# Optimization experiments

Measured on AMD Instinct MI355X. Metric: run time of the kernel, lower is better.

Reference implementation:

```python
import jax, jax.numpy as jnp
import numpy as np
import math

CHANNELS = 1024
NUM_HEADS = 16
HEAD_DIM = CHANNELS // NUM_HEADS  # 64
ROPE_DIM = int(HEAD_DIM * 0.5)    # 32
BASE_FREQ = 10000.0


def apply_rope(x):
    """x: [b, h, t, d]; rotate first ROPE_DIM features, pass the rest through."""
    t = x.shape[2]
    half = ROPE_DIM // 2
    theta = 1.0 / (BASE_FREQ ** (jnp.arange(0, ROPE_DIM, 2, dtype=jnp.float32) / ROPE_DIM))  # [half]
    ang = jnp.arange(t, dtype=jnp.float32)[:, None] * theta[None, :]  # [t, half]
    ang = jnp.concatenate([ang, ang], axis=-1)  # [t, ROPE_DIM]
    cos = jnp.cos(ang)[None, None, :, :]
    sin = jnp.sin(ang)[None, None, :, :]
    x_rope, x_pass = x[..., :ROPE_DIM], x[..., ROPE_DIM:]
    neg_half = jnp.concatenate([-x_rope[..., half:], x_rope[..., :half]], axis=-1)
    x_rope = x_rope * cos + neg_half * sin
    return jnp.concatenate([x_rope, x_pass], axis=-1)


def proximal_bias(length):
    pos = jnp.arange(length, dtype=jnp.float32)
    diff = pos[None, :] - pos[:, None]
    return -jnp.log1p(jnp.abs(diff))[None, None, :, :]  # [1,1,t,t]


def conv1x1(x, w, b):
    """x: [b, c_in, t], w: [c_out, c_in], b: [c_out] -> [b, c_out, t]"""
    return jnp.einsum('oc,bct->bot', w, x) + b[None, :, None]


def setup_inputs() -> dict:
    key = jax.random.key(0)
    ks = jax.random.split(key, 10)
    B, C, T = 8, CHANNELS, 1024
    scale = 1.0 / math.sqrt(C)
    return {
        "x": jax.random.normal(ks[0], (B, C, T), dtype=jnp.float32),
        "context": jax.random.normal(ks[1], (B, C, T), dtype=jnp.float32),
        "attention_mask": jnp.ones((B, 1, 1, T), dtype=jnp.int32),
        "Wq": jax.random.normal(ks[2], (C, C), dtype=jnp.float32) * scale,
        "bq": jnp.zeros((C,), dtype=jnp.float32),
        "Wk": jax.random.normal(ks[3], (C, C), dtype=jnp.float32) * scale,
        "bk": jnp.zeros((C,), dtype=jnp.float32),
        "Wv": jax.random.normal(ks[4], (C, C), dtype=jnp.float32) * scale,
        "bv": jnp.zeros((C,), dtype=jnp.float32),
        "Wo": jax.random.normal(ks[5], (C, C), dtype=jnp.float32) * scale,
        "bo": jnp.zeros((C,), dtype=jnp.float32),
    }


def reference(x, context, attention_mask, Wq, bq, Wk, bk, Wv, bv, Wo, bo):
    B, C, T = x.shape
    H, D = NUM_HEADS, HEAD_DIM
    q = conv1x1(x, Wq, bq)
    k = conv1x1(context, Wk, bk)
    v = conv1x1(context, Wv, bv)
    # b (h d) t -> b h t d
    def split_heads(z):
        return z.reshape(B, H, D, -1).transpose(0, 1, 3, 2)
    q, k, v = split_heads(q), split_heads(k), split_heads(v)
    q = apply_rope(q)
    k = apply_rope(k)
    scores = jnp.einsum('bhqd,bhkd->bhqk', q, k) / math.sqrt(D)
    scores = scores + proximal_bias(T)  # proximal_bias=True, self-attention
    scores = jnp.where(attention_mask == 0, jnp.float32(-10000.0), scores)
    probs = jax.nn.softmax(scores, axis=-1)  # dropout_rate=0.0 -> identity
    out = jnp.einsum('bhqk,bhkd->bhqd', probs, v)
    # b h q d -> b (h d) q
    out = out.transpose(0, 1, 3, 2).reshape(B, C, T)
    return conv1x1(out, Wo, bo)
```

## Files before the change

kernel.cpp:

```cpp
#include <hip/hip_runtime.h>
#include <hip/hip_bf16.h>
#include <math.h>

#define BB 8
#define CC 1024
#define TT 1024
#define HH 16
#define DD 64

typedef __attribute__((ext_vector_type(8))) short short8;
typedef __attribute__((ext_vector_type(4))) short short4_;
typedef __attribute__((ext_vector_type(4))) float f32x4;
typedef __attribute__((ext_vector_type(4))) int   i32x4;
typedef __attribute__((ext_vector_type(2))) unsigned long long u64x2;

#define QSCALE 0.18033688f

__device__ __forceinline__ unsigned short f2bf(float f) {
    unsigned u = __builtin_bit_cast(unsigned, f);
    u += 0x7fffu + ((u >> 16) & 1u);
    return (unsigned short)(u >> 16);
}

__device__ __forceinline__ f32x4 mfma16(short8 a, short8 b, f32x4 c) {
    return __builtin_amdgcn_mfma_f32_16x16x32_bf16(a, b, c, 0, 0, 0);
}

__device__ __forceinline__ void async16(const void* g, void* l) {
    __builtin_amdgcn_global_load_lds(
        (const __attribute__((address_space(1))) unsigned int*)g,
        (__attribute__((address_space(3))) unsigned int*)l, 16, 0, 0);
}

__device__ __forceinline__ unsigned cvtpk(float lo, float hi) {
    unsigned r;
    asm("v_cvt_pk_bf16_f32 %0, %1, %2" : "=v"(r) : "v"(lo), "v"(hi));
    return r;
}

__device__ __forceinline__ short8 vfrag(const short* p) {
    u64x2 t;
    t[0] = *(const unsigned long long*)(p);
    t[1] = *(const unsigned long long*)(p + 16);
    return __builtin_bit_cast(short8, t);
}

__global__ __launch_bounds__(256) void cast_w_kernel(
    const float* __restrict__ Wq, const float* __restrict__ Wk,
    const float* __restrict__ Wv, const float* __restrict__ Wo,
    unsigned short* __restrict__ dst)
{
    const int z = blockIdx.y;
    const float* W = (z == 0) ? Wq : (z == 1) ? Wk : (z == 2) ? Wv : Wo;
    unsigned short* d = dst + (size_t)z * CC * CC;
    int idx = blockIdx.x * 256 + threadIdx.x;
    float4 f = ((const float4*)W)[idx];
    short4_ s;
    s[0] = (short)f2bf(f.x); s[1] = (short)f2bf(f.y);
    s[2] = (short)f2bf(f.z); s[3] = (short)f2bf(f.w);
    ((short4_*)d)[idx] = s;
}

__global__ __launch_bounds__(256) void tcast2_kernel(
    const float* __restrict__ x, const float* __restrict__ ctx,
    unsigned short* __restrict__ xT, unsigned short* __restrict__ cTo)
{
    __shared__ float sT[64][65];
    const int tid = threadIdx.x;
    const int z = blockIdx.z;
    const float* in = (z < BB) ? x : ctx;
    unsigned short* out = (z < BB) ? xT : cTo;
    const int b = (z < BB) ? z : z - BB;
    const int tB = blockIdx.x * 64, cT = blockIdx.y * 64;

    const float* ib = in + ((size_t)b * CC + cT) * TT + tB;
    const int r = tid >> 2;
    #pragma unroll
    for (int j = 0; j < 4; j++) {
        int t4 = (tid & 3) * 4 + j * 16;
        float4 f = *(const float4*)(ib + (size_t)r * TT + t4);
        sT[r][t4 + 0] = f.x; sT[r][t4 + 1] = f.y;
        sT[r][t4 + 2] = f.z; sT[r][t4 + 3] = f.w;
    }
    __syncthreads();
    const int t_l = tid >> 2, cch = (tid & 3) * 16;
    short8 o0, o1;
    #pragma unroll
    for (int i = 0; i < 8; i++) {
        o0[i] = (short)f2bf(sT[cch + i][t_l]);
        o1[i] = (short)f2bf(sT[cch + 8 + i][t_l]);
    }
    unsigned short* dp = out + ((size_t)b * TT + tB + t_l) * CC + cT + cch;
    *(short8*)dp = o0;
    *(short8*)(dp + 8) = o1;
}

__global__ __launch_bounds__(256) void tcast_kernel(
    const float* __restrict__ in, unsigned short* __restrict__ out)
{
    __shared__ float sT[64][65];
    const int tid = threadIdx.x;
    const int tB = blockIdx.x * 64, cT = blockIdx.y * 64, b = blockIdx.z;

    const float* ib = in + ((size_t)b * CC + cT) * TT + tB;
    const int r = tid >> 2;
    #pragma unroll
    for (int j = 0; j < 4; j++) {
        int t4 = (tid & 3) * 4 + j * 16;
        float4 f = *(const float4*)(ib + (size_t)r * TT + t4);
        sT[r][t4 + 0] = f.x; sT[r][t4 + 1] = f.y;
        sT[r][t4 + 2] = f.z; sT[r][t4 + 3] = f.w;
    }
    __syncthreads();
    const int t_l = tid >> 2, cch = (tid & 3) * 16;
    short8 o0, o1;
    #pragma unroll
    for (int i = 0; i < 8; i++) {
        o0[i] = (short)f2bf(sT[cch + i][t_l]);
        o1[i] = (short)f2bf(sT[cch + 8 + i][t_l]);
    }
    unsigned short* dp = out + ((size_t)b * TT + tB + t_l) * CC + cT + cch;
    *(short8*)dp = o0;
    *(short8*)(dp + 8) = o1;
}

__global__ __launch_bounds__(256) void qkv_gll_kernel(
    const unsigned short* __restrict__ xT, const unsigned short* __restrict__ cT,
    const unsigned short* __restrict__ Wq2, const unsigned short* __restrict__ Wk2,
    const unsigned short* __restrict__ Wv2,
    const float* __restrict__ bq, const float* __restrict__ bk,
    const float* __restrict__ bv,
    unsigned short* __restrict__ qo, unsigned short* __restrict__ ko,
    unsigned short* __restrict__ vo,
    int mode)
{
    __shared__ __align__(16) short smem[4 * 64 * 72];
    short* sA = smem;
    short* sB = smem + 4096;

    const int tid = threadIdx.x, lane = tid & 63, wave = tid >> 6;
    const int wm = wave >> 1, wn = wave & 1;
    const int l15 = lane & 15, lq = lane >> 4;

    const int tTile = blockIdx.x, oTile = blockIdx.y;
    const int zz = blockIdx.z;
    int w, b;
    if (mode == 0)      { w = zz % 3;        b = zz / 3;  }
    else if (mode == 1) { w = 0;             b = zz;      }
    else                { w = 1 + (zz & 1);  b = zz >> 1; }
    const unsigned short* inT = (w == 0) ? xT : cT;
    const int oBase = oTile * 128, tBase = tTile * 128;

    const unsigned short* WA = (w == 0) ? Wq2 : (w == 1) ? Wk2 : Wv2;
    const float* bias        = (w == 0) ? bq  : (w == 1) ? bk  : bv;

    const int srow = lane >> 2;
    const int sch  = (lane ^ (lane >> 2) ^ (lane >> 4)) & 3;
    const unsigned short* gA0 = WA + (size_t)(oBase + wave * 32 + srow) * CC + sch * 8;
    const unsigned short* gA1 = gA0 + (size_t)16 * CC;
    const unsigned short* gB0 = inT + ((size_t)b * TT + tBase + wave * 32 + srow) * CC + sch * 8;
    const unsigned short* gB1 = gB0 + (size_t)16 * CC;
    short* lA0 = sA + (wave * 2 + 0) * 512;
    short* lA1 = sA + (wave * 2 + 1) * 512;
    short* lB0 = sB + (wave * 2 + 0) * 512;
    short* lB1 = sB + (wave * 2 + 1) * 512;

    const int csw = ((lq ^ (l15 & 3) ^ (l15 >> 2)) & 3) * 8;

    f32x4 acc[4][4];
    #pragma unroll
    for (int mt = 0; mt < 4; mt++)
        #pragma unroll
        for (int nt = 0; nt < 4; nt++) acc[mt][nt] = (f32x4){0.f, 0.f, 0.f, 0.f};

    for (int c0 = 0; c0 < CC; c0 += 32) {
        async16(gA0 + c0, lA0);
        async16(gA1 + c0, lA1);
        async16(gB0 + c0, lB0);
        async16(gB1 + c0, lB1);
        __syncthreads();

        short8 af[4], bf[4];
        #pragma unroll
        for (int mt = 0; mt < 4; mt++)
            af[mt] = *(short8*)(sA + (wm * 64 + mt * 16 + l15) * 32 + csw);
        #pragma unroll
        for (int nt = 0; nt < 4; nt++)
            bf[nt] = *(short8*)(sB + (wn * 64 + nt * 16 + l15) * 32 + csw);
        #pragma unroll
        for (int mt = 0; mt < 4; mt++)
            #pragma unroll
            for (int nt = 0; nt < 4; nt++)
                acc[mt][nt] = mfma16(af[mt], bf[nt], acc[mt][nt]);
        __syncthreads();
    }

    #pragma unroll
    for (int mt = 0; mt < 4; mt++)
        #pragma unroll
        for (int r = 0; r < 4; r++) {
            float bi = bias[oBase + wm * 64 + mt * 16 + lq * 4 + r];
            #pragma unroll
            for (int nt = 0; nt < 4; nt++) {
                acc[mt][nt][r] += bi;
                if (w == 0) acc[mt][nt][r] *= QSCALE;
            }
        }

    const int h = oTile * 2 + wm;
    short* sT = smem + wave * (64 * 72);

    if (w < 2) {
        #pragma unroll
        for (int r = 0; r < 4; r++) {
            float dr = (float)(lq * 4 + r);
            float theta = exp2f(dr * -0.8304820237f);
            float sa, ca, ss, cs;
            sincosf((float)(tBase + wn * 64 + l15) * theta, &sa, &ca);
            sincosf(16.0f * theta, &ss, &cs);
            #pragma unroll
            for (int nt = 0; nt < 4; nt++) {
                float x0 = acc[0][nt][r], x1 = acc[1][nt][r];
                acc[0][nt][r] = x0 * ca - x1 * sa;
                acc[1][nt][r] = x1 * ca + x0 * sa;
                float c2 = ca * cs - sa * ss;
                sa = sa * cs + ca * ss;
                ca = c2;
            }
        }
        #pragma unroll
        for (int nt = 0; nt < 4; nt++)
            #pragma unroll
            for (int mt = 0; mt < 4; mt++) {
                short4_ v4;
                #pragma unroll
                for (int r = 0; r < 4; r++) v4[r] = (short)f2bf(acc[mt][nt][r]);
                *(short4_*)(sT + (nt * 16 + l15) * 72 + mt * 16 + lq * 4) = v4;
            }
    } else {
        #pragma unroll
        for (int mt = 0; mt < 4; mt++)
            #pragma unroll
            for (int r = 0; r < 4; r++)
                #pragma unroll
                for (int nt = 0; nt < 4; nt++)
                    sT[(mt * 16 + lq * 4 + r) * 72 + nt * 16 + l15] =
                        (short)f2bf(acc[mt][nt][r]);
    }
    __asm__ volatile("s_waitcnt lgkmcnt(0)" ::: "memory");

    unsigned short* dstBase;
    if (w == 0)
        dstBase = qo + ((size_t)(b * HH + h) * TT + tBase + wn * 64 + lane) * DD;
    else if (w == 1)
        dstBase = ko + ((size_t)(b * HH + h) * TT + tBase + wn * 64 + lane) * DD;
    else
        dstBase = vo + ((size_t)(b * HH + h) * DD + lane) * TT + tBase + wn * 64;
    #pragma unroll
    for (int j = 0; j < 8; j++)
        *(short8*)(dstBase + j * 8) = *(short8*)(sT + lane * 72 + j * 8);
}

__global__ __launch_bounds__(256) void oproj_gll_kernel(
    const unsigned short* __restrict__ att, const unsigned short* __restrict__ Wo2,
    const float* __restrict__ bo, float* __restrict__ out)
{
    __shared__ __align__(16) short smem[8192];
    short* sA = smem;
    short* sB = smem + 4096;

    const int tid = threadIdx.x, lane = tid & 63, wave = tid >> 6;
    const int wm = wave >> 1, wn = wave & 1;
    const int l15 = lane & 15, lq = lane >> 4;
    const int tTile = blockIdx.x, oTile = blockIdx.y, b = blockIdx.z;
    const int oBase = oTile * 128, tBase = tTile * 128;

    const int srow = lane >> 2;
    const int sch  = (lane ^ (lane >> 2) ^ (lane >> 4)) & 3;
    const unsigned short* gA0 = Wo2 + (size_t)(oBase + wave * 32 + srow) * CC + sch * 8;
    const unsigned short* gA1 = gA0 + (size_t)16 * CC;
    const unsigned short* attB = att + (size_t)b * HH * TT * DD;
    const int t0 = tBase + wave * 32 + srow;
    short* lA0 = sA + (wave * 2 + 0) * 512;
    short* lA1 = sA + (wave * 2 + 1) * 512;
    short* lB0 = sB + (wave * 2 + 0) * 512;
    short* lB1 = sB + (wave * 2 + 1) * 512;

    const int csw = ((lq ^ (l15 & 3) ^ (l15 >> 2)) & 3) * 8;

    f32x4 acc[4][4];
    #pragma unroll
    for (int mt = 0; mt < 4; mt++)
        #pragma unroll
        for (int nt = 0; nt < 4; nt++) acc[mt][nt] = (f32x4){0.f, 0.f, 0.f, 0.f};

    for (int c0 = 0; c0 < CC; c0 += 32) {
        int c = c0 + sch * 8;
        const unsigned short* g0 =
            attB + ((size_t)(c >> 6) * TT + t0) * DD + (c & 63);
        async16(gA0 + c0, lA0);
        async16(gA1 + c0, lA1);
        async16(g0, lB0);
        async16(g0 + 16 * DD, lB1);
        __syncthreads();

        short8 af[4], bf[4];
        #pragma unroll
        for (int mt = 0; mt < 4; mt++)
            af[mt] = *(short8*)(sA + (wm * 64 + mt * 16 + l15) * 32 + csw);
        #pragma unroll
        for (int nt = 0; nt < 4; nt++)
            bf[nt] = *(short8*)(sB + (wn * 64 + nt * 16 + l15) * 32 + csw);
        #pragma unroll
        for (int mt = 0; mt < 4; mt++)
            #pragma unroll
            for (int nt = 0; nt < 4; nt++)
                acc[mt][nt] = mfma16(af[mt], bf[nt], acc[mt][nt]);
        __syncthreads();
    }

    #pragma unroll
    for (int mt = 0; mt < 4; mt++)
        #pragma unroll
        for (int r = 0; r < 4; r++) {
            int o = oBase + wm * 64 + mt * 16 + lq * 4 + r;
            float bi = bo[o];
            float* dst = out + ((size_t)b * CC + o) * TT + tBase + wn * 64;
            #pragma unroll
            for (int nt = 0; nt < 4; nt++)
                dst[nt * 16 + l15] = acc[mt][nt][r] + bi;
        }
}

__global__ __launch_bounds__(256) void attn_mfma_kernel(
    const unsigned short* __restrict__ q, const unsigned short* __restrict__ k,
    const unsigned short* __restrict__ v, const int* __restrict__ mask,
    unsigned short* __restrict__ att)
{
    __shared__ __align__(16) short sQw[64 * 72];
    __shared__ __align__(16) short sK[64 * 72];
    __shared__ __align__(16) short sV[64 * 72];

    const int tid = threadIdx.x, lane = tid & 63, wq = tid >> 6;
    const int l15 = lane & 15, lq = lane >> 4;
    const int qTile = blockIdx.x, bh = blockIdx.y, b = bh >> 4;

    const int sr = tid >> 2, sc = (tid & 3) * 16;

    {
        const unsigned short* gq = q + ((size_t)bh * TT + qTile * 64 + sr) * DD + sc;
        *(short8*)(sQw + sr * 72 + sc)     = *(const short8*)gq;
        *(short8*)(sQw + sr * 72 + sc + 8) = *(const short8*)(gq + 8);
    }
    __syncthreads();

    const short8 bq0 = *(short8*)(sQw + (wq * 16 + l15) * 72 + lq * 8);
    const short8 bq1 = *(short8*)(sQw + (wq * 16 + l15) * 72 + 32 + lq * 8);
    __syncthreads();

    float* wtab = (float*)sQw;
    #pragma unroll
    for (int j = 0; j < 8; j++) {
        int d = tid + 256 * j;
        int ad = d - 1023; ad = ad < 0 ? -ad : ad;
        wtab[d] = __builtin_amdgcn_rcpf(1.0f + (float)ad);
    }

    f32x4 accO[4];
    #pragma unroll
    for (int nt = 0; nt < 4; nt++) accO[nt] = (f32x4){0.f, 0.f, 0.f, 0.f};
    float l_sum = 0.f;

    const int qpos = qTile * 64 + wq * 16 + l15;
    const int* maskB = mask + b * TT;
    const unsigned short* kB = k + (size_t)bh * TT * DD;
    const unsigned short* vB = v + (size_t)bh * DD * TT;

    const unsigned short* gk = kB + (size_t)sr * DD + sc;
    const unsigned short* gv = vB + (size_t)sr * TT + sc;
    short8 kr0 = *(const short8*)gk;
    short8 kr1 = *(const short8*)(gk + 8);
    short8 vr0 = *(const short8*)gv;
    short8 vr1 = *(const short8*)(gv + 8);

    for (int kt = 0; kt < 16; kt++) {
        __syncthreads();
        *(short8*)(sK + sr * 72 + sc)     = kr0;
        *(short8*)(sK + sr * 72 + sc + 8) = kr1;
        *(short8*)(sV + sr * 72 + sc)     = vr0;
        *(short8*)(sV + sr * 72 + sc + 8) = vr1;
        __syncthreads();

        if (kt < 15) {
            gk += 64 * DD;
            gv += 64;
            kr0 = *(const short8*)gk;
            kr1 = *(const short8*)(gk + 8);
            vr0 = *(const short8*)gv;
            vr1 = *(const short8*)(gv + 8);
        }

        f32x4 s4[4];
        #pragma unroll
        for (int nt = 0; nt < 4; nt++) {
            short8 ka0 = *(short8*)(sK + (nt * 16 + l15) * 72 + lq * 8);
            short8 ka1 = *(short8*)(sK + (nt * 16 + l15) * 72 + 32 + lq * 8);
            f32x4 z = (f32x4){0.f, 0.f, 0.f, 0.f};
            z = mfma16(ka0, bq0, z);
            z = mfma16(ka1, bq1, z);
            s4[nt] = z;
        }

        const float* wrow = wtab + (kt * 64 + lq * 4 + 1023 - qpos);
        unsigned pk8[4][2];
        #pragma unroll
        for (int nt = 0; nt < 4; nt++) {
            i32x4 mk = *(const i32x4*)(maskB + kt * 64 + nt * 16 + lq * 4);
            #pragma unroll
            for (int h2 = 0; h2 < 2; h2++) {
                float p0 = exp2f(s4[nt][2 * h2])     * wrow[nt * 16 + 2 * h2];
                float p1 = exp2f(s4[nt][2 * h2 + 1]) * wrow[nt * 16 + 2 * h2 + 1];
                p0 = mk[2 * h2]     ? p0 : 0.f;
                p1 = mk[2 * h2 + 1] ? p1 : 0.f;
                l_sum += p0 + p1;
                pk8[nt][h2] = cvtpk(p0, p1);
            }
        }

        i32x4 c0 = {(int)pk8[0][0], (int)pk8[0][1], (int)pk8[1][0], (int)pk8[1][1]};
        i32x4 c1 = {(int)pk8[2][0], (int)pk8[2][1], (int)pk8[3][0], (int)pk8[3][1]};
        short8 ap0 = __builtin_bit_cast(short8, c0);
        short8 ap1 = __builtin_bit_cast(short8, c1);

        #pragma unroll
        for (int nt = 0; nt < 4; nt++) {
            const short* vr = sV + (nt * 16 + l15) * 72 + lq * 4;
            short8 b0 = vfrag(vr);
            short8 b1 = vfrag(vr + 32);
            accO[nt] = mfma16(ap0, b0, accO[nt]);
            accO[nt] = mfma16(ap1, b1, accO[nt]);
        }
    }

    float tot = l_sum;
    tot += __shfl_xor(tot, 16);
    tot += __shfl_xor(tot, 32);

    unsigned short* aB = att + ((size_t)bh * TT + qTile * 64 + wq * 16 + lq * 4) * DD;
    #pragma unroll
    for (int r = 0; r < 4; r++) {
        float inv = 1.0f / __shfl(tot, lq * 4 + r);
        #pragma unroll
        for (int nt = 0; nt < 4; nt++)
            aB[(size_t)r * DD + nt * 16 + l15] = f2bf(accO[nt][r] * inv);
    }
}

__global__ __launch_bounds__(256) void qkv_mfma_kernel(
    const float* __restrict__ x, const float* __restrict__ ctx,
    const float* __restrict__ Wq, const float* __restrict__ bq,
    const float* __restrict__ Wk, const float* __restrict__ bk,
    const float* __restrict__ Wv, const float* __restrict__ bv,
    unsigned short* __restrict__ qo, unsigned short* __restrict__ ko,
    unsigned short* __restrict__ vo)
{
    __shared__ __align__(16) short smem[4 * 64 * 72];
    short* sA = smem;
    short* sB = smem + 128 * 40;

    const int tid  = threadIdx.x;
    const int lane = tid & 63;
    const int wave = tid >> 6;
    const int wm = wave >> 1, wn = wave & 1;
    const int l15 = lane & 15, lq = lane >> 4;

    const int tTile = blockIdx.x, oTile = blockIdx.y;
    const int b = blockIdx.z / 3, w = blockIdx.z % 3;
    const int oBase = oTile * 128, tBase = tTile * 128;

    const float* In   = (w == 0) ? x  : ctx;
    const float* W    = (w == 0) ? Wq : (w == 1) ? Wk : Wv;
    const float* bias = (w == 0) ? bq : (w == 1) ? bk : bv;
    const float* InB  = In + (size_t)b * CC * TT;

    const int ao = tid >> 1, ak = (tid & 1) * 16;
    const int bt = tid & 127, bk_ = (tid >> 7) * 16;
    const float* gA = W + (size_t)(oBase + ao) * CC + ak;
    const float* gB = InB + (size_t)bk_ * TT + tBase + bt;

    f32x4 acc[4][4];
    #pragma unroll
    for (int mt = 0; mt < 4; mt++)
        #pragma unroll
        for (int nt = 0; nt < 4; nt++) acc[mt][nt] = (f32x4){0.f, 0.f, 0.f, 0.f};

    for (int c0 = 0; c0 < CC; c0 += 32) {
        float fa[16], fb[16];
        #pragma unroll
        for (int i = 0; i < 4; i++) {
            float4 t4 = *(const float4*)(gA + c0 + 4 * i);
            fa[4*i+0] = t4.x; fa[4*i+1] = t4.y; fa[4*i+2] = t4.z; fa[4*i+3] = t4.w;
        }
        #pragma unroll
        for (int j = 0; j < 16; j++)
            fb[j] = gB[(size_t)(c0 + j) * TT];

        __syncthreads();
        short8 pa0, pa1, pb0, pb1;
        #pragma unroll
        for (int e = 0; e < 8; e++) {
            pa0[e] = (short)f2bf(fa[e]);   pa1[e] = (short)f2bf(fa[8 + e]);
            pb0[e] = (short)f2bf(fb[e]);   pb1[e] = (short)f2bf(fb[8 + e]);
        }
        *(short8*)(sA + ao * 40 + ak)     = pa0;
        *(short8*)(sA + ao * 40 + ak + 8) = pa1;
        *(short8*)(sB + bt * 40 + bk_)     = pb0;
        *(short8*)(sB + bt * 40 + bk_ + 8) = pb1;
        __syncthreads();

        short8 af[4], bf[4];
        #pragma unroll
        for (int mt = 0; mt < 4; mt++)
            af[mt] = *(short8*)(sA + (wm * 64 + mt * 16 + l15) * 40 + lq * 8);
        #pragma unroll
        for (int nt = 0; nt < 4; nt++)
            bf[nt] = *(short8*)(sB + (wn * 64 + nt * 16 + l15) * 40 + lq * 8);
        #pragma unroll
        for (int mt = 0; mt < 4; mt++)
            #pragma unroll
            for (int nt = 0; nt < 4; nt++)
                acc[mt][nt] = mfma16(af[mt], bf[nt], acc[mt][nt]);
    }

    #pragma unroll
    for (int mt = 0; mt < 4; mt++)
        #pragma unroll
        for (int r = 0; r < 4; r++) {
            float bi = bias[oBase + wm * 64 + mt * 16 + lq * 4 + r];
            #pragma unroll
            for (int nt = 0; nt < 4; nt++) {
                acc[mt][nt][r] += bi;
                if (w == 0) acc[mt][nt][r] *= QSCALE;
            }
        }

    const int h = oTile * 2 + wm;
    __syncthreads();
    short* sT = smem + wave * (64 * 72);

    if (w < 2) {
        #pragma unroll
        for (int r = 0; r < 4; r++) {
            float theta = powf(10000.0f, -(float)(lq * 4 + r) * (1.0f / 16.0f));
            #pragma unroll
            for (int nt = 0; nt < 4; nt++) {
                float tpos = (float)(tBase + wn * 64 + nt * 16 + l15);
                float sa, ca;
                sincosf(tpos * theta, &sa, &ca);
                float x0 = acc[0][nt][r], x1 = acc[1][nt][r];
                acc[0][nt][r] = x0 * ca - x1 * sa;
                acc[1][nt][r] = x1 * ca + x0 * sa;
            }
        }
        #pragma unroll
        for (int nt = 0; nt < 4; nt++)
            #pragma unroll
            for (int mt = 0; mt < 4; mt++) {
                short4_ v4;
                #pragma unroll
                for (int r = 0; r < 4; r++) v4[r] = (short)f2bf(acc[mt][nt][r]);
                *(short4_*)(sT + (nt * 16 + l15) * 72 + mt * 16 + lq * 4) = v4;
            }
    } else {
        #pragma unroll
        for (int mt = 0; mt < 4; mt++)
            #pragma unroll
            for (int r = 0; r < 4; r++)
                #pragma unroll
                for (int nt = 0; nt < 4; nt++)
                    sT[(mt * 16 + lq * 4 + r) * 72 + nt * 16 + l15] =
                        (short)f2bf(acc[mt][nt][r]);
    }
    __asm__ volatile("s_waitcnt lgkmcnt(0)" ::: "memory");

    unsigned short* dstBase;
    if (w == 0)
        dstBase = qo + ((size_t)(b * HH + h) * TT + tBase + wn * 64 + lane) * DD;
    else if (w == 1)
        dstBase = ko + ((size_t)(b * HH + h) * TT + tBase + wn * 64 + lane) * DD;
    else
        dstBase = vo + ((size_t)(b * HH + h) * DD + lane) * TT + tBase + wn * 64;
    #pragma unroll
    for (int j = 0; j < 8; j++)
        *(short8*)(dstBase + j * 8) = *(short8*)(sT + lane * 72 + j * 8);
}

__global__ __launch_bounds__(256) void oproj_mfma_kernel(
    const unsigned short* __restrict__ att, const float* __restrict__ Wo,
    const float* __restrict__ bo, float* __restrict__ out)
{
    __shared__ __align__(16) short smem[2 * 128 * 40];
    short* sA = smem;
    short* sB = smem + 128 * 40;

    const int tid = threadIdx.x, lane = tid & 63, wave = tid >> 6;
    const int wm = wave >> 1, wn = wave & 1;
    const int l15 = lane & 15, lq = lane >> 4;
    const int tTile = blockIdx.x, oTile = blockIdx.y, b = blockIdx.z;
    const int oBase = oTile * 128, tBase = tTile * 128;

    const int ao = tid >> 1, ak = (tid & 1) * 16;
    const int bt = tid & 127, bk_ = (tid >> 7) * 16;
    const float* gA = Wo + (size_t)(oBase + ao) * CC + ak;

    f32x4 acc[4][4];
    #pragma unroll
    for (int mt = 0; mt < 4; mt++)
        #pragma unroll
        for (int nt = 0; nt < 4; nt++) acc[mt][nt] = (f32x4){0.f, 0.f, 0.f, 0.f};

    for (int c0 = 0; c0 < CC; c0 += 32) {
        float fa[16];
        #pragma unroll
        for (int i = 0; i < 4; i++) {
            float4 t4 = *(const float4*)(gA + c0 + 4 * i);
            fa[4*i+0] = t4.x; fa[4*i+1] = t4.y; fa[4*i+2] = t4.z; fa[4*i+3] = t4.w;
        }
        int c = c0 + bk_;
        const unsigned short* gB =
            att + (((size_t)b * HH + (c >> 6)) * TT + tBase + bt) * DD + (c & 63);
        short8 pb0 = *(const short8*)gB;
        short8 pb1 = *(const short8*)(gB + 8);

        __syncthreads();
        short8 pa0, pa1;
        #pragma unroll
        for (int e = 0; e < 8; e++) {
            pa0[e] = (short)f2bf(fa[e]); pa1[e] = (short)f2bf(fa[8 + e]);
        }
        *(short8*)(sA + ao * 40 + ak)      = pa0;
        *(short8*)(sA + ao * 40 + ak + 8)  = pa1;
        *(short8*)(sB + bt * 40 + bk_)     = pb0;
        *(short8*)(sB + bt * 40 + bk_ + 8) = pb1;
        __syncthreads();

        short8 af[4], bf[4];
        #pragma unroll
        for (int mt = 0; mt < 4; mt++)
            af[mt] = *(short8*)(sA + (wm * 64 + mt * 16 + l15) * 40 + lq * 8);
        #pragma unroll
        for (int nt = 0; nt < 4; nt++)
            bf[nt] = *(short8*)(sB + (wn * 64 + nt * 16 + l15) * 40 + lq * 8);
        #pragma unroll
        for (int mt = 0; mt < 4; mt++)
            #pragma unroll
            for (int nt = 0; nt < 4; nt++)
                acc[mt][nt] = mfma16(af[mt], bf[nt], acc[mt][nt]);
    }

    #pragma unroll
    for (int mt = 0; mt < 4; mt++)
        #pragma unroll
        for (int r = 0; r < 4; r++) {
            int o = oBase + wm * 64 + mt * 16 + lq * 4 + r;
            float bi = bo[o];
            float* dst = out + ((size_t)b * CC + o) * TT + tBase + wn * 64;
            #pragma unroll
            for (int nt = 0; nt < 4; nt++)
                dst[nt * 16 + l15] = acc[mt][nt][r] + bi;
        }
}

extern "C" void kernel_launch(void* const* d_in, const int* in_sizes, int n_in,
                              void* d_out, int out_size, void* d_ws, size_t ws_size,
                              hipStream_t stream)
{
    const float* x   = (const float*)d_in[0];
    const float* ctx = (const float*)d_in[1];
    const int* mask  = (const int*)d_in[2];
    const float* Wq  = (const float*)d_in[3];
    const float* bq  = (const float*)d_in[4];
    const float* Wk  = (const float*)d_in[5];
    const float* bk  = (const float*)d_in[6];
    const float* Wv  = (const float*)d_in[7];
    const float* bv  = (const float*)d_in[8];
    const float* Wo  = (const float*)d_in[9];
    const float* bo  = (const float*)d_in[10];
    float* out = (float*)d_out;

    const size_t nq = (size_t)BB * HH * TT * DD;
    const size_t nw = (size_t)CC * CC;

    if (ws_size >= (5 * nq + 4 * nw) * sizeof(unsigned short)) {
        unsigned short* q   = (unsigned short*)d_ws;
        unsigned short* k   = q + nq;
        unsigned short* v   = k + nq;
        unsigned short* xT  = v + nq;
        unsigned short* cT  = xT + nq;
        unsigned short* Wb  = cT + nq;
        unsigned short* Wqb = Wb;
        unsigned short* Wkb = Wb + nw;
        unsigned short* Wvb = Wb + 2 * nw;
        unsigned short* Wob = Wb + 3 * nw;

        cast_w_kernel<<<dim3(1024, 4), 256, 0, stream>>>(Wq, Wk, Wv, Wo, Wb);
        tcast2_kernel<<<dim3(16, 16, BB * 2), 256, 0, stream>>>(x, ctx, xT, cT);
        qkv_gll_kernel<<<dim3(8, 8, BB * 3), 256, 0, stream>>>(
            xT, cT, Wqb, Wkb, Wvb, bq, bk, bv, q, k, v, 0);
        attn_mfma_kernel<<<dim3(TT / 64, BB * HH), 256, 0, stream>>>(
            q, k, v, mask, xT);
        oproj_gll_kernel<<<dim3(8, 8, BB), 256, 0, stream>>>(xT, Wob, bo, out);
    } else if (ws_size >= (4 * nq + 4 * nw) * sizeof(unsigned short)) {
        unsigned short* q   = (unsigned short*)d_ws;
        unsigned short* k   = q + nq;
        unsigned short* v   = k + nq;
        unsigned short* buf = v + nq;
        unsigned short* Wb  = buf + nq;
        unsigned short* Wqb = Wb;
        unsigned short* Wkb = Wb + nw;
        unsigned short* Wvb = Wb + 2 * nw;
        unsigned short* Wob = Wb + 3 * nw;

        cast_w_kernel<<<dim3(1024, 4), 256, 0, stream>>>(Wq, Wk, Wv, Wo, Wb);
        tcast_kernel<<<dim3(16, 16, BB), 256, 0, stream>>>(x, buf);
        qkv_gll_kernel<<<dim3(8, 8, BB), 256, 0, stream>>>(
            buf, buf, Wqb, Wkb, Wvb, bq, bk, bv, q, k, v, 1);
        tcast_kernel<<<dim3(16, 16, BB), 256, 0, stream>>>(ctx, buf);
        qkv_gll_kernel<<<dim3(8, 8, BB * 2), 256, 0, stream>>>(
            buf, buf, Wqb, Wkb, Wvb, bq, bk, bv, q, k, v, 2);
        attn_mfma_kernel<<<dim3(TT / 64, BB * HH), 256, 0, stream>>>(
            q, k, v, mask, buf);
        oproj_gll_kernel<<<dim3(8, 8, BB), 256, 0, stream>>>(buf, Wob, bo, out);
    } else {
        unsigned short* q   = (unsigned short*)d_ws;
        unsigned short* k   = q + nq;
        unsigned short* v   = k + nq;
        unsigned short* att = v + nq;
        qkv_mfma_kernel<<<dim3(8, 8, BB * 3), 256, 0, stream>>>(
            x, ctx, Wq, bq, Wk, bk, Wv, bv, q, k, v);
        attn_mfma_kernel<<<dim3(TT / 64, BB * HH), 256, 0, stream>>>(
            q, k, v, mask, att);
        oproj_mfma_kernel<<<dim3(8, 8, BB), 256, 0, stream>>>(att, Wo, bo, out);
    }
}
```

Before: 330.0 us.

## Hoist mask check, compute softmax denominator via MFMA, permute V smem layout

Adds a block-wide check on whether the attention mask is all ones and, when it is, skips the per-tile mask loads and selects. The row sum of probabilities is now computed by an extra MFMA against a vector of bf16 ones instead of scalar adds followed by shuffles. The denominator therefore uses the bf16-rounded probabilities, which matches the values fed to the PV MFMA. V is written into shared memory in a permuted 8-byte layout so the B fragments are read with two 16-byte loads instead of four 8-byte loads. exp2f is replaced by the hardware exp2 intrinsic. The costs are one extra MFMA pair per key tile and a small mask scan at kernel start.

```diff
diff --git a/kernel.cpp b/kernel.cpp
--- a/kernel.cpp
+++ b/kernel.cpp
@@ -36,13 +36,6 @@
     unsigned r;
     asm("v_cvt_pk_bf16_f32 %0, %1, %2" : "=v"(r) : "v"(lo), "v"(hi));
     return r;
-}
-
-__device__ __forceinline__ short8 vfrag(const short* p) {
-    u64x2 t;
-    t[0] = *(const unsigned long long*)(p);
-    t[1] = *(const unsigned long long*)(p + 16);
-    return __builtin_bit_cast(short8, t);
 }
 
 __global__ __launch_bounds__(256) void cast_w_kernel(
@@ -340,12 +333,21 @@
     __shared__ __align__(16) short sQw[64 * 72];
     __shared__ __align__(16) short sK[64 * 72];
     __shared__ __align__(16) short sV[64 * 72];
+    __shared__ int sOK[4];
 
     const int tid = threadIdx.x, lane = tid & 63, wq = tid >> 6;
     const int l15 = lane & 15, lq = lane >> 4;
     const int qTile = blockIdx.x, bh = blockIdx.y, b = bh >> 4;
 
     const int sr = tid >> 2, sc = (tid & 3) * 16;
+    const int* maskB = mask + b * TT;
+
+    {
+        i32x4 m4 = *(const i32x4*)(maskB + tid * 4);
+        int ok = (m4[0] != 0) & (m4[1] != 0) & (m4[2] != 0) & (m4[3] != 0);
+        unsigned long long bal = __ballot(ok);
+        if (lane == 0) sOK[wq] = (bal == ~0ull);
+    }
 
     {
         const unsigned short* gq = q + ((size_t)bh * TT + qTile * 64 + sr) * DD + sc;
@@ -356,6 +358,7 @@
 
     const short8 bq0 = *(short8*)(sQw + (wq * 16 + l15) * 72 + lq * 8);
     const short8 bq1 = *(short8*)(sQw + (wq * 16 + l15) * 72 + 32 + lq * 8);
+    const bool allOK = sOK[0] && sOK[1] && sOK[2] && sOK[3];
     __syncthreads();
 
     float* wtab = (float*)sQw;
@@ -366,15 +369,21 @@
         wtab[d] = __builtin_amdgcn_rcpf(1.0f + (float)ad);
     }
 
+    short8 vones;
+    #pragma unroll
+    for (int e = 0; e < 8; e++) vones[e] = (short)0x3F80;
+
     f32x4 accO[4];
     #pragma unroll
     for (int nt = 0; nt < 4; nt++) accO[nt] = (f32x4){0.f, 0.f, 0.f, 0.f};
-    float l_sum = 0.f;
+    f32x4 accD = (f32x4){0.f, 0.f, 0.f, 0.f};
 
     const int qpos = qTile * 64 + wq * 16 + l15;
-    const int* maskB = mask + b * TT;
     const unsigned short* kB = k + (size_t)bh * TT * DD;
     const unsigned short* vB = v + (size_t)bh * DD * TT;
+
+    const int xo = ((tid & 3) >> 1) * 8 + (tid & 1) * 4;
+    short* vwp = sV + sr * 72 + xo;
 
     const unsigned short* gk = kB + (size_t)sr * DD + sc;
     const unsigned short* gv = vB + (size_t)sr * TT + sc;
@@ -387,8 +396,14 @@
         __syncthreads();
         *(short8*)(sK + sr * 72 + sc)     = kr0;
         *(short8*)(sK + sr * 72 + sc + 8) = kr1;
-        *(short8*)(sV + sr * 72 + sc)     = vr0;
-        *(short8*)(sV + sr * 72 + sc + 8) = vr1;
+        {
+            u64x2 vv0 = __builtin_bit_cast(u64x2, vr0);
+            u64x2 vv1 = __builtin_bit_cast(u64x2, vr1);
+            *(unsigned long long*)(vwp)      = vv0[0];
+            *(unsigned long long*)(vwp + 16) = vv0[1];
+            *(unsigned long long*)(vwp + 32) = vv1[0];
+            *(unsigned long long*)(vwp + 48) = vv1[1];
+        }
         __syncthreads();
 
         if (kt < 15) {
@@ -413,17 +428,32 @@
 
         const float* wrow = wtab + (kt * 64 + lq * 4 + 1023 - qpos);
         unsigned pk8[4][2];
-        #pragma unroll
-        for (int nt = 0; nt < 4; nt++) {
-            i32x4 mk = *(const i32x4*)(maskB + kt * 64 + nt * 16 + lq * 4);
-            #pragma unroll
-            for (int h2 = 0; h2 < 2; h2++) {
-                float p0 = exp2f(s4[nt][2 * h2])     * wrow[nt * 16 + 2 * h2];
-                float p1 = exp2f(s4[nt][2 * h2 + 1]) * wrow[nt * 16 + 2 * h2 + 1];
-                p0 = mk[2 * h2]     ? p0 : 0.f;
-                p1 = mk[2 * h2 + 1] ? p1 : 0.f;
-                l_sum += p0 + p1;
-                pk8[nt][h2] = cvtpk(p0, p1);
+        if (allOK) {
+            #pragma unroll
+            for (int nt = 0; nt < 4; nt++) {
+                #pragma unroll
+                for (int h2 = 0; h2 < 2; h2++) {
+                    float p0 = __builtin_amdgcn_exp2f(s4[nt][2 * h2])
+                               * wrow[nt * 16 + 2 * h2];
+                    float p1 = __builtin_amdgcn_exp2f(s4[nt][2 * h2 + 1])
+                               * wrow[nt * 16 + 2 * h2 + 1];
+                    pk8[nt][h2] = cvtpk(p0, p1);
+                }
+            }
+        } else {
+            #pragma unroll
+            for (int nt = 0; nt < 4; nt++) {
+                i32x4 mk = *(const i32x4*)(maskB + kt * 64 + nt * 16 + lq * 4);
+                #pragma unroll
+                for (int h2 = 0; h2 < 2; h2++) {
+                    float p0 = __builtin_amdgcn_exp2f(s4[nt][2 * h2])
+                               * wrow[nt * 16 + 2 * h2];
+                    float p1 = __builtin_amdgcn_exp2f(s4[nt][2 * h2 + 1])
+                               * wrow[nt * 16 + 2 * h2 + 1];
+                    p0 = mk[2 * h2]     ? p0 : 0.f;
+                    p1 = mk[2 * h2 + 1] ? p1 : 0.f;
+                    pk8[nt][h2] = cvtpk(p0, p1);
+                }
             }
         }
 
@@ -432,24 +462,23 @@
         short8 ap0 = __builtin_bit_cast(short8, c0);
         short8 ap1 = __builtin_bit_cast(short8, c1);
 
+        accD = mfma16(ap0, vones, accD);
+        accD = mfma16(ap1, vones, accD);
+
         #pragma unroll
         for (int nt = 0; nt < 4; nt++) {
-            const short* vr = sV + (nt * 16 + l15) * 72 + lq * 4;
-            short8 b0 = vfrag(vr);
-            short8 b1 = vfrag(vr + 32);
+            const short* vrow = sV + (nt * 16 + l15) * 72 + lq * 16;
+            short8 b0 = *(short8*)(vrow);
+            short8 b1 = *(short8*)(vrow + 8);
             accO[nt] = mfma16(ap0, b0, accO[nt]);
             accO[nt] = mfma16(ap1, b1, accO[nt]);
         }
     }
 
-    float tot = l_sum;
-    tot += __shfl_xor(tot, 16);
-    tot += __shfl_xor(tot, 32);
-
     unsigned short* aB = att + ((size_t)bh * TT + qTile * 64 + wq * 16 + lq * 4) * DD;
     #pragma unroll
     for (int r = 0; r < 4; r++) {
-        float inv = 1.0f / __shfl(tot, lq * 4 + r);
+        float inv = 1.0f / accD[r];
         #pragma unroll
         for (int nt = 0; nt < 4; nt++)
             aB[(size_t)r * DD + nt * 16 + l15] = f2bf(accO[nt][r] * inv);
```

After: 304.1 us. 7.8% less time.
